# Optimization experiments

Measured on AMD Instinct MI355X. Metric: run time of the kernel, lower is better.

## Reference

```python
import jax, jax.numpy as jnp
import numpy as np

NUM_TAGS = 64
BSZ = 256
SEQ_LEN = 2048


def setup_inputs() -> dict:
    key = jax.random.key(0)
    k1, k2, k3, k4, k5 = jax.random.split(key, 5)
    inputs = jax.random.normal(k1, (BSZ, SEQ_LEN, NUM_TAGS), dtype=jnp.float32)
    tags = jax.random.randint(k2, (BSZ, SEQ_LEN), 0, NUM_TAGS, dtype=jnp.int32)
    mask = jnp.ones((BSZ, SEQ_LEN), dtype=jnp.int32)
    # parameters (xavier-normal-ish transitions, normal start/end)
    std = float(np.sqrt(2.0 / (NUM_TAGS + NUM_TAGS)))
    transitions = jax.random.normal(k3, (NUM_TAGS, NUM_TAGS), dtype=jnp.float32) * std
    start_transitions = jax.random.normal(k4, (NUM_TAGS,), dtype=jnp.float32)
    end_transitions = jax.random.normal(k5, (NUM_TAGS,), dtype=jnp.float32)
    return {"inputs": inputs, "tags": tags, "mask": mask,
            "transitions": transitions,
            "start_transitions": start_transitions,
            "end_transitions": end_transitions}


def _input_likelihood(logits, maskf, transitions, start_transitions, end_transitions):
    # logits: (B, S, T); maskf: (B, S) float
    logits_t = jnp.transpose(logits, (1, 0, 2))   # (S, B, T)
    mask_t = maskf.T                               # (S, B)
    alpha0 = start_transitions[None, :] + logits_t[0]  # (B, T)

    def step(alpha, xs):
        emit, m = xs  # emit: (B, T), m: (B,)
        # inner[b, i, j] = alpha[b, i] + transitions[i, j] + emit[b, j]
        inner = alpha[:, :, None] + transitions[None, :, :] + emit[:, None, :]
        new_alpha = jax.nn.logsumexp(inner, axis=1)  # (B, T)
        alpha = new_alpha * m[:, None] + alpha * (1.0 - m[:, None])
        return alpha, None

    alpha, _ = jax.lax.scan(step, alpha0, (logits_t[1:], mask_t[1:]))
    stops = alpha + end_transitions[None, :]
    return jax.nn.logsumexp(stops, axis=-1)  # (B,)


def _joint_likelihood(logits, tags, mask, maskf, transitions, start_transitions, end_transitions):
    # logits: (B, S, T); tags, mask: (B, S)
    B = logits.shape[0]
    tags = tags * mask  # zero out padded positions
    score = start_transitions[tags[:, 0]]  # (B,)
    # transition scores for t -> t+1, masked by mask[t+1]
    trans = transitions[tags[:, :-1], tags[:, 1:]] * maskf[:, 1:]  # (B, S-1)
    # emission scores for t in [0, S-2], masked by mask[t]
    emit = jnp.take_along_axis(logits[:, :-1, :], tags[:, :-1, None], axis=2)[..., 0]
    emit = emit * maskf[:, :-1]  # (B, S-1)
    score = score + trans.sum(axis=1) + emit.sum(axis=1)
    # last valid tag
    last_idx = maskf.sum(axis=1).astype(jnp.int32) - 1  # (B,)
    batch_ar = jnp.arange(B)
    last_tags = tags[batch_ar, last_idx]  # (B,)
    last_transition_score = end_transitions[last_tags]
    last_input_score = logits[:, -1, :][batch_ar, last_tags]  # (B,)
    score = score + last_transition_score + last_input_score * maskf[:, -1]
    return score  # (B,)


def reference(inputs, tags, mask, transitions, start_transitions, end_transitions):
    maskf = mask.astype(jnp.float32)
    log_denominator = _input_likelihood(inputs, maskf, transitions,
                                        start_transitions, end_transitions)
    log_numerator = _joint_likelihood(inputs, tags, mask, maskf, transitions,
                                      start_transitions, end_transitions)
    return jnp.sum(log_numerator - log_denominator)
```

## Files before the change

kernel.cpp:

```cpp
#include <hip/hip_runtime.h>

#define BSZ 256
#define SEQ 2048
#define NT  64
#define KS  5.0f

#define CLT 8
#define SC  (16 * CLT)
#define NG  (SEQ / SC)

#define SROW  136
#define SSLAB (16 * SROW + 8)
#define RWS   68

typedef __fp16 half2_t __attribute__((ext_vector_type(2)));
typedef __fp16 half4_t __attribute__((ext_vector_type(4)));
typedef float  f32x4_t __attribute__((ext_vector_type(4)));
typedef int    int2_t  __attribute__((ext_vector_type(2)));

static __device__ __forceinline__ float wave_red_sum(float x) {
#pragma unroll
    for (int d = 1; d < 64; d <<= 1) x += __shfl_xor(x, d);
    return x;
}

static __device__ __forceinline__ float dpp_xor1(float v) {
    return __builtin_bit_cast(float,
        __builtin_amdgcn_update_dpp(0, __builtin_bit_cast(int, v), 0xB1, 0xF, 0xF, true));
}
static __device__ __forceinline__ float dpp_xor2(float v) {
    return __builtin_bit_cast(float,
        __builtin_amdgcn_update_dpp(0, __builtin_bit_cast(int, v), 0x4E, 0xF, 0xF, true));
}

static __device__ __forceinline__ half4_t pack4(float a, float b, float c, float d) {
    half2_t lo = __builtin_amdgcn_cvt_pkrtz(a, b);
    half2_t hi = __builtin_amdgcn_cvt_pkrtz(c, d);
    int2_t t;
    t.x = __builtin_bit_cast(int, lo);
    t.y = __builtin_bit_cast(int, hi);
    return __builtin_bit_cast(half4_t, t);
}

__global__ __launch_bounds__(128) void crf_pre_kernel(
    const float* __restrict__ trans,
    half4_t* __restrict__ EtabF,
    half4_t* __restrict__ EtabB)
{
    for (int e = threadIdx.x; e < 1024; e += 128) {
        int lane = e & 63, slot = e >> 6;
        int q = slot >> 2, kc = slot & 3;
        int rlo = lane & 15, h = lane >> 4;
        int m = 16 * q + rlo;
        float f[4], bb[4];
#pragma unroll
        for (int i = 0; i < 4; ++i) {
            int k = 16 * kc + 4 * h + i;
            f[i]  = __expf(trans[k * NT + m]);
            bb[i] = __expf(trans[m * NT + k]);
        }
        EtabF[e] = pack4(f[0], f[1], f[2], f[3]);
        EtabB[e] = pack4(bb[0], bb[1], bb[2], bb[3]);
    }
}

__global__ __launch_bounds__(128) void crf_fat_kernel(
    const float* __restrict__ logits,
    const int*   __restrict__ tags,
    const int*   __restrict__ mask,
    const float* __restrict__ trans,
    const float* __restrict__ startT,
    const float* __restrict__ endT,
    const half4_t* __restrict__ EtabF,
    const half4_t* __restrict__ EtabB,
    float* __restrict__ rB,
    float* __restrict__ wB,
    float* __restrict__ Jpart,
    float* __restrict__ numtrans)
{
    __shared__ __align__(16) unsigned char Flds[CLT * SSLAB];
    __shared__ int lmbits[16];

    if (blockIdx.x < BSZ) {
        const int b   = blockIdx.x;
        const int tid = threadIdx.x;
        float* redf = (float*)Flds;
        int*   redi = (int*)(Flds + 512);

        const int*   __restrict__ tg = tags + (size_t)b * SEQ;
        const int*   __restrict__ mk = mask + (size_t)b * SEQ;
        const float* __restrict__ Lr = logits + (size_t)b * SEQ * NT;

        float acc = 0.0f;
        int   cnt = 0;
        for (int t = tid; t < SEQ; t += 128) {
            int mt  = mk[t];
            cnt += mt;
            int tgt = tg[t] * mt;
            if (t < SEQ - 1) {
                int m1 = mk[t + 1];
                acc += trans[tgt * NT + tg[t + 1] * m1] * (float)m1;
                acc += Lr[t * NT + tgt] * (float)mt;
            }
        }
        redf[tid] = acc;
        redi[tid] = cnt;
        __syncthreads();
        for (int off = 64; off > 0; off >>= 1) {
            if (tid < off) {
                redf[tid] += redf[tid + off];
                redi[tid] += redi[tid + off];
            }
            __syncthreads();
        }
        if (tid == 0) {
            int   last_idx = redi[0] - 1;
            int   m_last   = mk[SEQ - 1];
            int   tag0     = tg[0] * mk[0];
            int   last_tag = tg[last_idx] * mk[last_idx];
            float r = redf[0] + startT[tag0] + endT[last_tag];
            r += Lr[(size_t)(SEQ - 1) * NT + last_tag] * (float)m_last;
            numtrans[b] = r;
        }
        return;
    }

    const int blk  = blockIdx.x - BSZ;
    const int b    = blk / NG;
    const int g    = blk % NG;
    const int tid  = threadIdx.x;
    const bool fwd = (tid >> 6) == 0;
    const int lane = tid & 63;
    const int rlo  = lane & 15;
    const int h    = lane >> 4;

    const float* __restrict__ Lg = logits + ((size_t)b * SEQ + (size_t)g * SC) * NT;
#pragma unroll
    for (int hh = 0; hh < 2; ++hh) {
        f32x4_t xb[8];
#pragma unroll
        for (int jj = 0; jj < 8; ++jj) {
            int gci = (hh * 8 + jj) * 128 + tid;
            xb[jj] = *(const f32x4_t*)(Lg + (size_t)(gci >> 4) * NT + (gci & 15) * 4);
        }
#pragma unroll
        for (int jj = 0; jj < 8; ++jj) {
            int gci = (hh * 8 + jj) * 128 + tid;
            int row = gci >> 4;
            int col = gci & 15;
            int k   = row / CLT;
            int s   = row % CLT;
            half2_t p0 = __builtin_amdgcn_cvt_pkrtz(__expf(xb[jj][0] - KS), __expf(xb[jj][1] - KS));
            half2_t p1 = __builtin_amdgcn_cvt_pkrtz(__expf(xb[jj][2] - KS), __expf(xb[jj][3] - KS));
            int2_t w;
            w.x = __builtin_bit_cast(int, p0);
            w.y = __builtin_bit_cast(int, p1);
            *(int2_t*)(Flds + s * SSLAB + k * SROW + col * 8) = w;
        }
    }
    if (tid < 16) {
        const int* mk = mask + (size_t)b * SEQ + (size_t)g * SC + tid * CLT;
        int bits = 0;
#pragma unroll
        for (int s = 0; s < CLT; ++s) bits |= (mk[s] ? 1 : 0) << s;
        if (g == 0 && tid == 0) bits &= ~1;
        lmbits[tid] = bits;
    }

    const half4_t* __restrict__ Et = fwd ? EtabF : EtabB;
    half4_t A[4][4];
#pragma unroll
    for (int q = 0; q < 4; ++q)
#pragma unroll
        for (int kc = 0; kc < 4; ++kc)
            A[q][kc] = Et[(q * 4 + kc) * 64 + lane];

    __syncthreads();

    const int mbits = lmbits[rlo];
    f32x4_t V[4];
    float C = KS * (float)__builtin_popcount(mbits);
#pragma unroll
    for (int q = 0; q < 4; ++q)
#pragma unroll
        for (int i = 0; i < 4; ++i) V[q][i] = 1.0f;

    if (fwd && g == 0 && rlo == 0) {
        float mx = -1e30f;
        f32x4_t al[4];
#pragma unroll
        for (int q = 0; q < 4; ++q) {
            f32x4_t em = *(const f32x4_t*)(logits + (size_t)b * SEQ * NT + 16 * q + 4 * h);
            f32x4_t st = *(const f32x4_t*)(startT + 16 * q + 4 * h);
#pragma unroll
            for (int i = 0; i < 4; ++i) {
                al[q][i] = st[i] + em[i];
                mx = fmaxf(mx, al[q][i]);
            }
        }
        mx = fmaxf(mx, __shfl_xor(mx, 16));
        mx = fmaxf(mx, __shfl_xor(mx, 32));
        C += mx;
#pragma unroll
        for (int q = 0; q < 4; ++q)
#pragma unroll
            for (int i = 0; i < 4; ++i) V[q][i] = __expf(al[q][i] - mx);
    }

    const unsigned char* Fbase = Flds + rlo * SROW + h * 8;

    if (fwd) {
#pragma unroll
        for (int s = 0; s < CLT; ++s) {
            half4_t Fh[4];
#pragma unroll
            for (int q = 0; q < 4; ++q)
                Fh[q] = *(const half4_t*)(Fbase + s * SSLAB + q * 32);
            half4_t Xh[4];
#pragma unroll
            for (int kc = 0; kc < 4; ++kc)
                Xh[kc] = pack4(V[kc][0], V[kc][1], V[kc][2], V[kc][3]);
            f32x4_t Y[4];
#pragma unroll
            for (int q = 0; q < 4; ++q) {
                f32x4_t a0 = {0.0f, 0.0f, 0.0f, 0.0f};
                f32x4_t a1 = {0.0f, 0.0f, 0.0f, 0.0f};
                a0 = __builtin_amdgcn_mfma_f32_16x16x16f16(A[q][0], Xh[0], a0, 0, 0, 0);
                a0 = __builtin_amdgcn_mfma_f32_16x16x16f16(A[q][1], Xh[1], a0, 0, 0, 0);
                a1 = __builtin_amdgcn_mfma_f32_16x16x16f16(A[q][2], Xh[2], a1, 0, 0, 0);
                a1 = __builtin_amdgcn_mfma_f32_16x16x16f16(A[q][3], Xh[3], a1, 0, 0, 0);
                Y[q] = a0 + a1;
            }
            int mt = (mbits >> s) & 1;
#pragma unroll
            for (int q = 0; q < 4; ++q)
#pragma unroll
                for (int i = 0; i < 4; ++i) {
                    float w = Y[q][i] * (float)Fh[q][i];
                    V[q][i] = mt ? w : V[q][i];
                }
        }
    } else {
#pragma unroll
        for (int s = CLT - 1; s >= 0; --s) {
            half4_t Fh[4];
#pragma unroll
            for (int kc = 0; kc < 4; ++kc)
                Fh[kc] = *(const half4_t*)(Fbase + s * SSLAB + kc * 32);
            half4_t Xh[4];
#pragma unroll
            for (int kc = 0; kc < 4; ++kc)
                Xh[kc] = pack4(V[kc][0] * (float)Fh[kc][0],
                               V[kc][1] * (float)Fh[kc][1],
                               V[kc][2] * (float)Fh[kc][2],
                               V[kc][3] * (float)Fh[kc][3]);
            f32x4_t Y[4];
#pragma unroll
            for (int q = 0; q < 4; ++q) {
                f32x4_t a0 = {0.0f, 0.0f, 0.0f, 0.0f};
                f32x4_t a1 = {0.0f, 0.0f, 0.0f, 0.0f};
                a0 = __builtin_amdgcn_mfma_f32_16x16x16f16(A[q][0], Xh[0], a0, 0, 0, 0);
                a0 = __builtin_amdgcn_mfma_f32_16x16x16f16(A[q][1], Xh[1], a0, 0, 0, 0);
                a1 = __builtin_amdgcn_mfma_f32_16x16x16f16(A[q][2], Xh[2], a1, 0, 0, 0);
                a1 = __builtin_amdgcn_mfma_f32_16x16x16f16(A[q][3], Xh[3], a1, 0, 0, 0);
                Y[q] = a0 + a1;
            }
            int mt = (mbits >> s) & 1;
#pragma unroll
            for (int q = 0; q < 4; ++q)
#pragma unroll
                for (int i = 0; i < 4; ++i)
                    V[q][i] = mt ? Y[q][i] : V[q][i];
        }
    }

    __syncthreads();
    float* Rarr = (float*)Flds;
    float* Warr = Rarr + 16 * RWS;
    {
        float* dst = (fwd ? Rarr : Warr) + rlo * RWS + 4 * h;
#pragma unroll
        for (int q = 0; q < 4; ++q) *(f32x4_t*)(dst + 16 * q) = V[q];
    }
    __syncthreads();

    if (fwd) {
        const int c   = lane >> 2;
        const int sub = lane & 3;
        float dot = 0.0f, rho = 0.0f;
        {
            const float* br = Rarr + (c == 0 ? 0 : (c - 1)) * RWS + sub * 16;
            const float* bw = Warr + c * RWS + sub * 16;
#pragma unroll
            for (int u = 0; u < 4; ++u) {
                f32x4_t rv = *(const f32x4_t*)(br + 4 * u);
                f32x4_t wv = *(const f32x4_t*)(bw + 4 * u);
#pragma unroll
                for (int i = 0; i < 4; ++i) {
                    dot = fmaf(rv[i], wv[i], dot);
                    rho += wv[i];
                }
            }
        }
        dot += dpp_xor1(dot); dot += dpp_xor2(dot);
        rho += dpp_xor1(rho); rho += dpp_xor2(rho);

        float part = 0.0f;
        if (c >= 1 && sub == 0) part = __logf(dot) - __logf(rho);
        if (h == 0) part += C;
        float tot = wave_red_sum(part);
        if (lane == 0) Jpart[b * NG + g] = tot;

        if (rlo == 15) {
            float* dst = rB + ((size_t)b * NG + g) * 64 + 4 * h;
#pragma unroll
            for (int q = 0; q < 4; ++q) *(f32x4_t*)(dst + 16 * q) = V[q];
        }
    } else {
        if (rlo == 0) {
            float* dst = wB + ((size_t)b * NG + g) * 64 + 4 * h;
#pragma unroll
            for (int q = 0; q < 4; ++q) *(f32x4_t*)(dst + 16 * q) = V[q];
        }
    }
}

__global__ __launch_bounds__(64) void crf_glue_kernel(
    const float* __restrict__ rB,
    const float* __restrict__ wB,
    const float* __restrict__ Jpart,
    const float* __restrict__ endT,
    float* __restrict__ den)
{
    const int b = blockIdx.x;
    const int j = threadIdx.x;

    float acc = (j < NG) ? Jpart[b * NG + j] : 0.0f;
    acc = wave_red_sum(acc);

    float part = 0.0f;
    for (int g = 1; g < NG; ++g) {
        float rv = rB[((size_t)b * NG + g - 1) * 64 + j];
        float wv = wB[((size_t)b * NG + g) * 64 + j];
        float dot = wave_red_sum(rv * wv);
        float rho = wave_red_sum(wv);
        part += __logf(dot) - __logf(rho);
    }
    float fin = wave_red_sum(rB[((size_t)b * NG + NG - 1) * 64 + j] * __expf(endT[j]));

    if (j == 0) den[b] = acc + part + __logf(fin);
}

__global__ __launch_bounds__(256) void crf_reduce_kernel(
    const float* __restrict__ den,
    const float* __restrict__ numtrans,
    float* __restrict__ out)
{
    __shared__ float red[256];
    const int tid = threadIdx.x;
    red[tid] = numtrans[tid] - den[tid];
    __syncthreads();
    for (int off = 128; off > 0; off >>= 1) {
        if (tid < off) red[tid] += red[tid + off];
        __syncthreads();
    }
    if (tid == 0) out[0] = red[0];
}

extern "C" void kernel_launch(void* const* d_in, const int* in_sizes, int n_in,
                              void* d_out, int out_size, void* d_ws, size_t ws_size,
                              hipStream_t stream)
{
    const float* logits = (const float*)d_in[0];
    const int*   tags   = (const int*)  d_in[1];
    const int*   mask   = (const int*)  d_in[2];
    const float* trans  = (const float*)d_in[3];
    const float* startT = (const float*)d_in[4];
    const float* endT   = (const float*)d_in[5];
    float* out = (float*)d_out;
    float* ws  = (float*)d_ws;

    float*   den      = ws;
    float*   numtrans = ws + BSZ;
    float*   Jpart    = ws + 2 * BSZ;
    float*   rB       = Jpart + (size_t)BSZ * NG;
    float*   wB       = rB + (size_t)BSZ * NG * 64;
    half4_t* EtabF    = (half4_t*)(wB + (size_t)BSZ * NG * 64);
    half4_t* EtabB    = EtabF + 1024;

    crf_pre_kernel<<<1, 128, 0, stream>>>(trans, EtabF, EtabB);
    crf_fat_kernel<<<BSZ + BSZ * NG, 128, 0, stream>>>(
        logits, tags, mask, trans, startT, endT, EtabF, EtabB, rB, wB, Jpart, numtrans);
    crf_glue_kernel<<<BSZ, 64, 0, stream>>>(rB, wB, Jpart, endT, den);
    crf_reduce_kernel<<<1, 256, 0, stream>>>(den, numtrans, out);
}
```

Before: 57.89 us.

## Fold pre and reduce kernels into fat and glue kernels, parallelize glue

Removes the separate precompute kernel: each fat-kernel block now computes the exp(transitions) fp16 tables directly from trans in registers. The glue kernel is rewritten so each group of four lanes handles one chunk boundary with vector loads and DPP reductions, in place of the serial loop over NG wave reductions. The final reduce kernel is replaced by a last-block-done atomic counter pattern, which needs a memset of the counter before launch. This cuts launch count and serialized glue work, at the cost of redundant exp work in every fat block and an extra memset.

```diff
diff --git a/kernel.cpp b/kernel.cpp
--- a/kernel.cpp
+++ b/kernel.cpp
@@ -42,28 +42,6 @@
     return __builtin_bit_cast(half4_t, t);
 }
 
-__global__ __launch_bounds__(128) void crf_pre_kernel(
-    const float* __restrict__ trans,
-    half4_t* __restrict__ EtabF,
-    half4_t* __restrict__ EtabB)
-{
-    for (int e = threadIdx.x; e < 1024; e += 128) {
-        int lane = e & 63, slot = e >> 6;
-        int q = slot >> 2, kc = slot & 3;
-        int rlo = lane & 15, h = lane >> 4;
-        int m = 16 * q + rlo;
-        float f[4], bb[4];
-#pragma unroll
-        for (int i = 0; i < 4; ++i) {
-            int k = 16 * kc + 4 * h + i;
-            f[i]  = __expf(trans[k * NT + m]);
-            bb[i] = __expf(trans[m * NT + k]);
-        }
-        EtabF[e] = pack4(f[0], f[1], f[2], f[3]);
-        EtabB[e] = pack4(bb[0], bb[1], bb[2], bb[3]);
-    }
-}
-
 __global__ __launch_bounds__(128) void crf_fat_kernel(
     const float* __restrict__ logits,
     const int*   __restrict__ tags,
@@ -71,8 +49,6 @@
     const float* __restrict__ trans,
     const float* __restrict__ startT,
     const float* __restrict__ endT,
-    const half4_t* __restrict__ EtabF,
-    const half4_t* __restrict__ EtabB,
     float* __restrict__ rB,
     float* __restrict__ wB,
     float* __restrict__ Jpart,
@@ -167,13 +143,20 @@
         lmbits[tid] = bits;
     }
 
-    const half4_t* __restrict__ Et = fwd ? EtabF : EtabB;
     half4_t A[4][4];
 #pragma unroll
     for (int q = 0; q < 4; ++q)
 #pragma unroll
-        for (int kc = 0; kc < 4; ++kc)
-            A[q][kc] = Et[(q * 4 + kc) * 64 + lane];
+        for (int kc = 0; kc < 4; ++kc) {
+            float e[4];
+#pragma unroll
+            for (int i = 0; i < 4; ++i) {
+                int m = 16 * q + rlo;
+                int k = 16 * kc + 4 * h + i;
+                e[i] = __expf(fwd ? trans[k * NT + m] : trans[m * NT + k]);
+            }
+            A[q][kc] = pack4(e[0], e[1], e[2], e[3]);
+        }
 
     __syncthreads();
 
@@ -330,41 +313,65 @@
     const float* __restrict__ wB,
     const float* __restrict__ Jpart,
     const float* __restrict__ endT,
-    float* __restrict__ den)
-{
-    const int b = blockIdx.x;
-    const int j = threadIdx.x;
-
-    float acc = (j < NG) ? Jpart[b * NG + j] : 0.0f;
-    acc = wave_red_sum(acc);
-
-    float part = 0.0f;
-    for (int g = 1; g < NG; ++g) {
-        float rv = rB[((size_t)b * NG + g - 1) * 64 + j];
-        float wv = wB[((size_t)b * NG + g) * 64 + j];
-        float dot = wave_red_sum(rv * wv);
-        float rho = wave_red_sum(wv);
-        part += __logf(dot) - __logf(rho);
-    }
-    float fin = wave_red_sum(rB[((size_t)b * NG + NG - 1) * 64 + j] * __expf(endT[j]));
-
-    if (j == 0) den[b] = acc + part + __logf(fin);
-}
-
-__global__ __launch_bounds__(256) void crf_reduce_kernel(
-    const float* __restrict__ den,
     const float* __restrict__ numtrans,
+    float* __restrict__ diffs,
+    int*   __restrict__ counter,
     float* __restrict__ out)
 {
-    __shared__ float red[256];
-    const int tid = threadIdx.x;
-    red[tid] = numtrans[tid] - den[tid];
+    const int b    = blockIdx.x;
+    const int lane = threadIdx.x;
+    const int c    = lane >> 2;
+    const int sub  = lane & 3;
+
+    float dot = 0.0f, rho = 0.0f;
+    if (c == 0) {
+        const float* br = rB + ((size_t)b * NG + NG - 1) * 64 + sub * 16;
+#pragma unroll
+        for (int u = 0; u < 4; ++u) {
+            f32x4_t rv = *(const f32x4_t*)(br + 4 * u);
+            f32x4_t ev = *(const f32x4_t*)(endT + sub * 16 + 4 * u);
+#pragma unroll
+            for (int i = 0; i < 4; ++i) dot = fmaf(rv[i], __expf(ev[i]), dot);
+        }
+    } else {
+        const float* br = rB + ((size_t)b * NG + c - 1) * 64 + sub * 16;
+        const float* bw = wB + ((size_t)b * NG + c) * 64 + sub * 16;
+#pragma unroll
+        for (int u = 0; u < 4; ++u) {
+            f32x4_t rv = *(const f32x4_t*)(br + 4 * u);
+            f32x4_t wv = *(const f32x4_t*)(bw + 4 * u);
+#pragma unroll
+            for (int i = 0; i < 4; ++i) {
+                dot = fmaf(rv[i], wv[i], dot);
+                rho += wv[i];
+            }
+        }
+    }
+    dot += dpp_xor1(dot); dot += dpp_xor2(dot);
+    rho += dpp_xor1(rho); rho += dpp_xor2(rho);
+
+    float part = 0.0f;
+    if (sub == 0) {
+        part = (c == 0) ? __logf(dot) : (__logf(dot) - __logf(rho));
+    }
+    float contrib = part + ((lane < NG) ? Jpart[b * NG + lane] : 0.0f);
+    float den = wave_red_sum(contrib);
+
+    __shared__ int slast;
+    if (lane == 0) {
+        diffs[b] = numtrans[b] - den;
+        __threadfence();
+        int old = atomicAdd(counter, 1);
+        slast = (old == BSZ - 1) ? 1 : 0;
+    }
     __syncthreads();
-    for (int off = 128; off > 0; off >>= 1) {
-        if (tid < off) red[tid] += red[tid + off];
-        __syncthreads();
-    }
-    if (tid == 0) out[0] = red[0];
+    if (slast) {
+        __threadfence();
+        float x = diffs[lane] + diffs[lane + 64] +
+                  diffs[lane + 128] + diffs[lane + 192];
+        float tot = wave_red_sum(x);
+        if (lane == 0) out[0] = tot;
+    }
 }
 
 extern "C" void kernel_launch(void* const* d_in, const int* in_sizes, int n_in,
@@ -380,17 +387,16 @@
     float* out = (float*)d_out;
     float* ws  = (float*)d_ws;
 
-    float*   den      = ws;
-    float*   numtrans = ws + BSZ;
-    float*   Jpart    = ws + 2 * BSZ;
-    float*   rB       = Jpart + (size_t)BSZ * NG;
-    float*   wB       = rB + (size_t)BSZ * NG * 64;
-    half4_t* EtabF    = (half4_t*)(wB + (size_t)BSZ * NG * 64);
-    half4_t* EtabB    = EtabF + 1024;
-
-    crf_pre_kernel<<<1, 128, 0, stream>>>(trans, EtabF, EtabB);
+    float* numtrans = ws;
+    float* diffs    = ws + BSZ;
+    float* Jpart    = ws + 2 * BSZ;
+    float* rB       = Jpart + (size_t)BSZ * NG;
+    float* wB       = rB + (size_t)BSZ * NG * 64;
+    int*   counter  = (int*)(wB + (size_t)BSZ * NG * 64);
+
+    hipMemsetAsync(counter, 0, sizeof(int), stream);
     crf_fat_kernel<<<BSZ + BSZ * NG, 128, 0, stream>>>(
-        logits, tags, mask, trans, startT, endT, EtabF, EtabB, rB, wB, Jpart, numtrans);
-    crf_glue_kernel<<<BSZ, 64, 0, stream>>>(rB, wB, Jpart, endT, den);
-    crf_reduce_kernel<<<1, 256, 0, stream>>>(den, numtrans, out);
-}
+        logits, tags, mask, trans, startT, endT, rB, wB, Jpart, numtrans);
+    crf_glue_kernel<<<BSZ, 64, 0, stream>>>(rB, wB, Jpart, endT, numtrans,
+                                            diffs, counter, out);
+}
```

After: 71.30 us. 23.2% more time.
